# Optimization experiments

Hardware: AMD Instinct MI355X
Metric: run time of the kernel (lower is better)

## Reference

```python
import jax, jax.numpy as jnp
import numpy as np

N, E, H, HEADS, L = 10000, 64000, 128, 8, 8
D = H // HEADS
CUTOFF = 5.0
EPS = 1e-5


def _xavier(key, shape):
    lim = float(np.sqrt(6.0 / (shape[0] + shape[1])))
    return jax.random.uniform(key, shape, minval=-lim, maxval=lim, dtype=jnp.float32)


def setup_inputs() -> dict:
    key = jax.random.key(0)
    ks = jax.random.split(key, 20)
    zeros = lambda *s: jnp.zeros(s, jnp.float32)
    return {
        "x": jax.random.normal(ks[0], (N, H), jnp.float32),
        "vec": 0.1 * jax.random.normal(ks[1], (N, L, H), jnp.float32),
        "f_ij": jax.random.normal(ks[2], (E, H), jnp.float32),
        "d_ij": jax.random.normal(ks[3], (E, L), jnp.float32),
        "r_ij": jax.random.uniform(ks[4], (E,), jnp.float32, 0.0, CUTOFF),
        "edge_index": jax.random.randint(ks[5], (2, E), 0, N),
        "ln_g": jnp.ones((H,), jnp.float32), "ln_b": zeros(H),
        "vln_w": jnp.ones((H,), jnp.float32),
        "W_vec": _xavier(ks[6], (H, 3 * H)),
        "W_q": _xavier(ks[7], (H, H)), "b_q": zeros(H),
        "W_k": _xavier(ks[8], (H, H)), "b_k": zeros(H),
        "W_v": _xavier(ks[9], (H, H)), "b_v": zeros(H),
        "W_dk": _xavier(ks[10], (H, H)), "b_dk": zeros(H),
        "W_dv": _xavier(ks[11], (H, H)), "b_dv": zeros(H),
        "W_s": _xavier(ks[12], (H, 2 * H)), "b_s": zeros(2 * H),
        "W_f": _xavier(ks[13], (H, H)), "b_f": zeros(H),
        "W_src": _xavier(ks[14], (H, H)),
        "W_trg": _xavier(ks[15], (H, H)),
        "W_o": _xavier(ks[16], (H, 3 * H)), "b_o": zeros(3 * H),
    }


def _layernorm(x, g, b):
    mu = jnp.mean(x, -1, keepdims=True)
    var = jnp.mean((x - mu) ** 2, -1, keepdims=True)
    return (x - mu) * jax.lax.rsqrt(var + EPS) * g + b


def _cutoff(r):
    # CosineCutoff: 0.5*(cos(pi*r/cutoff)+1) for r < cutoff
    return 0.5 * (jnp.cos(jnp.pi * r / CUTOFF) + 1.0) * (r < CUTOFF).astype(r.dtype)


def _vec_rejection(v, d):
    # v: [E, L, H], d: [E, L]; remove the component of v along d (per channel)
    proj = jnp.einsum("elh,el->eh", v, d)
    return v - proj[:, None, :] * d[:, :, None]


def reference(x, vec, f_ij, d_ij, r_ij, edge_index, ln_g, ln_b, vln_w, W_vec,
              W_q, b_q, W_k, b_k, W_v, b_v, W_dk, b_dk, W_dv, b_dv,
              W_s, b_s, W_f, b_f, W_src, W_trg, W_o, b_o):
    src, dst = edge_index[0], edge_index[1]  # j (source), i (target)
    x = _layernorm(x, ln_g, ln_b)
    vec = vec * vln_w  # VecLayerNorm with norm_type="none": identity norm * weight

    q = (x @ W_q + b_q).reshape(N, HEADS, D)
    k = (x @ W_k + b_k).reshape(N, HEADS, D)
    v = (x @ W_v + b_v).reshape(N, HEADS, D)
    dk = jax.nn.silu(f_ij @ W_dk + b_dk).reshape(E, HEADS, D)
    dv = jax.nn.silu(f_ij @ W_dv + b_dv).reshape(E, HEADS, D)

    vec1, vec2, vec3 = jnp.split(jnp.einsum("nlh,hk->nlk", vec, W_vec), 3, axis=-1)
    vec_dot = jnp.sum(vec1 * vec2, axis=1)  # [N, H]

    # ---- message (per edge) ----
    attn = jnp.sum(q[dst] * k[src] * dk, axis=-1)          # [E, HEADS]
    attn = jax.nn.silu(attn) * _cutoff(r_ij)[:, None]
    vm = (v[src] * dv * attn[:, :, None]).reshape(E, H)    # [E, H]
    s1, s2 = jnp.split(jax.nn.silu(vm @ W_s + b_s), 2, axis=-1)
    vec_m = vec[src] * s1[:, None, :] + s2[:, None, :] * d_ij[:, :, None]  # [E, L, H]

    # ---- aggregate (scatter-add to target nodes) ----
    x_agg = jax.ops.segment_sum(vm, dst, num_segments=N)       # [N, H]
    vec_agg = jax.ops.segment_sum(vec_m, dst, num_segments=N)  # [N, L, H]

    # ---- edge update ----
    w1 = _vec_rejection(jnp.einsum("elh,hk->elk", vec[dst], W_trg), d_ij)
    w2 = _vec_rejection(jnp.einsum("elh,hk->elk", vec[src], W_src), -d_ij)
    w_dot = jnp.sum(w1 * w2, axis=1)                       # [E, H]
    df_ij = jax.nn.silu(f_ij @ W_f + b_f) * w_dot

    # ---- node update ----
    o1, o2, o3 = jnp.split(x_agg @ W_o + b_o, 3, axis=-1)
    dx = vec_dot * o2 + o3
    dvec = vec3 * o1[:, None, :] + vec_agg
    return dx, dvec, df_ij
```

## Files before the change

### kernel.cpp

```cpp
#include <hip/hip_runtime.h>
#include <hip/hip_bf16.h>
#include <math.h>

#define N_NODES 10000
#define N_EDGES 64000
#define H 128
#define L 8
#define NL (N_NODES * L)

typedef __attribute__((ext_vector_type(4))) float f32x4;
typedef __attribute__((ext_vector_type(8))) __bf16 bf16x8;
typedef __attribute__((ext_vector_type(4))) __bf16 bf16x4;

__device__ __forceinline__ float silu_f(float x) { return x / (1.f + __expf(-x)); }

__global__ __launch_bounds__(256) void ln_kernel(const float* __restrict__ x,
                                                 const float* __restrict__ g,
                                                 const float* __restrict__ b,
                                                 __bf16* __restrict__ out, int n_nodes) {
  int wave = threadIdx.x >> 6;
  int lane = threadIdx.x & 63;
  int n = blockIdx.x * 4 + wave;
  if (n >= n_nodes) return;
  const float* xr = x + (size_t)n * H;
  float a0 = xr[lane], a1 = xr[lane + 64];
  float s = a0 + a1;
#pragma unroll
  for (int off = 32; off >= 1; off >>= 1) s += __shfl_xor(s, off, 64);
  float mu = s * (1.f / H);
  float d0 = a0 - mu, d1 = a1 - mu;
  float v = d0 * d0 + d1 * d1;
#pragma unroll
  for (int off = 32; off >= 1; off >>= 1) v += __shfl_xor(v, off, 64);
  float rstd = rsqrtf(v * (1.f / H) + 1e-5f);
  __bf16* orow = out + (size_t)n * H;
  orow[lane] = (__bf16)(d0 * rstd * g[lane] + b[lane]);
  orow[lane + 64] = (__bf16)(d1 * rstd * g[lane + 64] + b[lane + 64]);
}

__global__ __launch_bounds__(256) void vecw_kernel(const float* __restrict__ vec,
                                                   const float* __restrict__ w,
                                                   __bf16* __restrict__ out,
                                                   __bf16* __restrict__ vecwT) {
  int n = blockIdx.x * 2 + (threadIdx.x >> 7);
  int h = threadIdx.x & 127;
  float wl = w[h];
  const float* base = vec + (size_t)n * 1024 + h;
  __bf16* orow = out + (size_t)n * 1024 + h;
  bf16x8 pack;
#pragma unroll
  for (int l = 0; l < 8; ++l) {
    __bf16 bv = (__bf16)(base[l * 128] * wl);
    orow[l * 128] = bv;
    pack[l] = bv;
  }
  *(bf16x8*)(vecwT + (size_t)n * 1024 + h * 8) = pack;
}

__global__ __launch_bounds__(256) void gatherf2b_kernel(const float* __restrict__ in,
                                                        const int* __restrict__ elist,
                                                        __bf16* __restrict__ out) {
  int p = blockIdx.x * 8 + (threadIdx.x >> 5);
  int c = (threadIdx.x & 31) * 4;
  int e = elist[p];
  f32x4 a = *(const f32x4*)(in + (size_t)e * 128 + c);
  bf16x4 h;
  h[0] = (__bf16)a[0]; h[1] = (__bf16)a[1]; h[2] = (__bf16)a[2]; h[3] = (__bf16)a[3];
  *(bf16x4*)(out + (size_t)p * 128 + c) = h;
}

__global__ __launch_bounds__(256) void dgather_kernel(const float* __restrict__ d_ij,
                                                      const float* __restrict__ r_ij,
                                                      const int* __restrict__ elist,
                                                      float* __restrict__ d2,
                                                      float* __restrict__ r2) {
  int idx = blockIdx.x * 256 + threadIdx.x;
  int p = idx >> 3, j = idx & 7;
  int e = elist[p];
  d2[idx] = d_ij[(size_t)e * 8 + j];
  if (j == 0) r2[p] = r_ij[e];
}

__global__ __launch_bounds__(256) void wconv_kernel(
    const float* __restrict__ Wvec, const float* __restrict__ Wq, const float* __restrict__ Wk,
    const float* __restrict__ Wv, const float* __restrict__ Wdk, const float* __restrict__ Wdv,
    const float* __restrict__ Ws, const float* __restrict__ Wtrg, const float* __restrict__ Wsrc,
    const float* __restrict__ Wf, const float* __restrict__ Wo,
    const float* __restrict__ bq, const float* __restrict__ bk, const float* __restrict__ bv,
    const float* __restrict__ bdk, const float* __restrict__ bdv, const float* __restrict__ bf,
    __bf16* __restrict__ Wt, float* __restrict__ bqkv, float* __restrict__ bfm) {
  int bid = blockIdx.x;
  int t = threadIdx.x;
  if (bid >= 256) {
    if (bid == 256) {
      if (t < 128) { bqkv[t] = bq[t]; bqkv[128 + t] = bk[t]; bqkv[256 + t] = bv[t]; }
    } else {
      if (t < 128) { bfm[t] = bdk[t]; bfm[128 + t] = bdv[t]; bfm[256 + t] = bf[t]; }
    }
    return;
  }
  int ct = bid >> 2, kt = bid & 3;
  int gc0 = ct * 32;
  const float* W; int ldw, sc0;
  if      (gc0 < 384)  { W = Wvec; ldw = 384; sc0 = gc0; }
  else if (gc0 < 512)  { W = Wtrg; ldw = 128; sc0 = gc0 - 384; }
  else if (gc0 < 640)  { W = Wsrc; ldw = 128; sc0 = gc0 - 512; }
  else if (gc0 < 768)  { W = Wq;   ldw = 128; sc0 = gc0 - 640; }
  else if (gc0 < 896)  { W = Wk;   ldw = 128; sc0 = gc0 - 768; }
  else if (gc0 < 1024) { W = Wv;   ldw = 128; sc0 = gc0 - 896; }
  else if (gc0 < 1152) { W = Wdk;  ldw = 128; sc0 = gc0 - 1024; }
  else if (gc0 < 1280) { W = Wdv;  ldw = 128; sc0 = gc0 - 1152; }
  else if (gc0 < 1408) { W = Wf;   ldw = 128; sc0 = gc0 - 1280; }
  else if (gc0 < 1664) { W = Ws;   ldw = 256; sc0 = gc0 - 1408; }
  else                 { W = Wo;   ldw = 384; sc0 = gc0 - 1664; }
  __shared__ float tile[32][33];
  int tx = t & 31, ty = t >> 5;
#pragma unroll
  for (int i = 0; i < 4; ++i)
    tile[ty + i * 8][tx] = W[(size_t)(kt * 32 + ty + i * 8) * ldw + sc0 + tx];
  __syncthreads();
#pragma unroll
  for (int i = 0; i < 4; ++i)
    Wt[(size_t)(gc0 + ty + i * 8) * 128 + kt * 32 + tx] = (__bf16)tile[tx][ty + i * 8];
}

__global__ __launch_bounds__(256, 2) void vdot_gemm(const __bf16* __restrict__ A,
                                                    const __bf16* __restrict__ Bt,
                                                    float* __restrict__ vdot) {
  __shared__ __bf16 As[128 * 128];
  const int tid = threadIdx.x;
  const int lane = tid & 63;
  const int wave = tid >> 6;
  const int wm = wave >> 1, wn = wave & 1;
  const int row0 = blockIdx.x * 128;

#pragma unroll
  for (int i = 0; i < 8; ++i) {
    int c = tid + i * 256;
    int row = c >> 4, k8 = c & 15;
    int k8s = k8 ^ (row & 7);
    const __bf16* src = A + (size_t)(row0 + row) * 128 + k8s * 8;
    __builtin_amdgcn_global_load_lds((const __attribute__((address_space(1))) void*)src,
                                     (__attribute__((address_space(3))) void*)(As + c * 8),
                                     16, 0, 0);
  }
  __syncthreads();

  f32x4 pacc[4][4], acc[4][4];
#pragma unroll
  for (int mi = 0; mi < 4; ++mi)
#pragma unroll
    for (int ni = 0; ni < 4; ++ni) {
      pacc[mi][ni] = f32x4{0.f, 0.f, 0.f, 0.f};
      acc[mi][ni] = f32x4{0.f, 0.f, 0.f, 0.f};
    }
#pragma unroll
  for (int ct = 0; ct < 2; ++ct) {
    const __bf16* Bbase =
        Bt + ((size_t)(ct * 128 + wn * 64 + (lane & 15)) << 7) + ((lane >> 4) << 3);
#pragma unroll
    for (int ks = 0; ks < 4; ++ks) {
      bf16x8 b[4];
#pragma unroll
      for (int ni = 0; ni < 4; ++ni) b[ni] = *(const bf16x8*)(Bbase + (ni << 11) + (ks << 5));
      bf16x8 a[4];
#pragma unroll
      for (int mi = 0; mi < 4; ++mi) {
        int row = wm * 64 + mi * 16 + (lane & 15);
        int byte = (row * 256 + ks * 64 + ((lane >> 4) << 4)) ^ ((row & 7) << 4);
        a[mi] = *(const bf16x8*)((const char*)As + byte);
      }
      if (ct == 0) {
#pragma unroll
        for (int mi = 0; mi < 4; ++mi)
#pragma unroll
          for (int ni = 0; ni < 4; ++ni)
            pacc[mi][ni] =
                __builtin_amdgcn_mfma_f32_16x16x32_bf16(a[mi], b[ni], pacc[mi][ni], 0, 0, 0);
      } else {
#pragma unroll
        for (int mi = 0; mi < 4; ++mi)
#pragma unroll
          for (int ni = 0; ni < 4; ++ni)
            acc[mi][ni] =
                __builtin_amdgcn_mfma_f32_16x16x32_bf16(a[mi], b[ni], acc[mi][ni], 0, 0, 0);
      }
    }
  }
#pragma unroll
  for (int mi = 0; mi < 4; ++mi) {
#pragma unroll
    for (int ni = 0; ni < 4; ++ni) {
      float sr = pacc[mi][ni][0] * acc[mi][ni][0] + pacc[mi][ni][1] * acc[mi][ni][1] +
                 pacc[mi][ni][2] * acc[mi][ni][2] + pacc[mi][ni][3] * acc[mi][ni][3];
      sr += __shfl_xor(sr, 16, 64);
      if ((lane & 16) == 0) {
        int node = (row0 >> 3) + wm * 8 + mi * 2 + (lane >> 5);
        int col = wn * 64 + ni * 16 + (lane & 15);
        vdot[(size_t)node * 128 + col] = sr;
      }
    }
  }
}

template <typename CT>
__global__ __launch_bounds__(256, 3) void gemm_v9(const __bf16* __restrict__ A,
                                                  const __bf16* __restrict__ Bt,
                                                  const float* __restrict__ bias,
                                                  CT* __restrict__ C, int M, int nx, int ny,
                                                  int ldc, int act) {
  __shared__ __bf16 As[128 * 128];
  __bf16* Cs = As;
  const int bid = blockIdx.x;
  const int xi = bid & 7;
  const int rem = bid >> 3;
  const int y = rem % ny;
  const int x = (rem / ny) * 8 + xi;
  if (x >= nx) return;
  const int tid = threadIdx.x;
  const int lane = tid & 63;
  const int wave = tid >> 6;
  const int wm = wave >> 1, wn = wave & 1;
  const int row0 = x * 128;

#pragma unroll
  for (int i = 0; i < 8; ++i) {
    int c = tid + i * 256;
    int row = c >> 4, k8 = c & 15;
    int k8s = k8 ^ (row & 7);
    const __bf16* src = A + (size_t)(row0 + row) * 128 + k8s * 8;
    __builtin_amdgcn_global_load_lds((const __attribute__((address_space(1))) void*)src,
                                     (__attribute__((address_space(3))) void*)(As + c * 8),
                                     16, 0, 0);
  }
  __syncthreads();

  const __bf16* Bbase =
      Bt + ((size_t)(y * 128 + wn * 64 + (lane & 15)) << 7) + ((lane >> 4) << 3);
  bf16x8 b[4][4];
#pragma unroll
  for (int ks = 0; ks < 4; ++ks)
#pragma unroll
    for (int ni = 0; ni < 4; ++ni) b[ks][ni] = *(const bf16x8*)(Bbase + (ni << 11) + (ks << 5));

  f32x4 acc[4][4];
#pragma unroll
  for (int mi = 0; mi < 4; ++mi)
#pragma unroll
    for (int ni = 0; ni < 4; ++ni) acc[mi][ni] = f32x4{0.f, 0.f, 0.f, 0.f};

#pragma unroll
  for (int ks = 0; ks < 4; ++ks) {
    bf16x8 a[4];
#pragma unroll
    for (int mi = 0; mi < 4; ++mi) {
      int row = wm * 64 + mi * 16 + (lane & 15);
      int byte = (row * 256 + ks * 64 + ((lane >> 4) << 4)) ^ ((row & 7) << 4);
      a[mi] = *(const bf16x8*)((const char*)As + byte);
    }
#pragma unroll
    for (int mi = 0; mi < 4; ++mi)
#pragma unroll
      for (int ni = 0; ni < 4; ++ni)
        acc[mi][ni] =
            __builtin_amdgcn_mfma_f32_16x16x32_bf16(a[mi], b[ks][ni], acc[mi][ni], 0, 0, 0);
  }

  const int cstore = y * 128;
  if constexpr (sizeof(CT) == 2) {
#pragma unroll
    for (int p = 0; p < 2; ++p) {
      __syncthreads();
      int rl = (wm << 5) | ((lane >> 4) << 2);
#pragma unroll
      for (int q = 0; q < 2; ++q) {
        int mi = 2 * p + q;
#pragma unroll
        for (int ni = 0; ni < 4; ++ni) {
          int col = wn * 64 + ni * 16 + (lane & 15);
          float bv = bias ? bias[cstore + col] : 0.f;
#pragma unroll
          for (int r = 0; r < 4; ++r) {
            float xv = acc[mi][ni][r] + bv;
            if (act) xv = silu_f(xv);
            Cs[(rl + q * 16 + r) * 136 + col] = (__bf16)xv;
          }
        }
      }
      __syncthreads();
#pragma unroll
      for (int rr = 0; rr < 4; ++rr) {
        int row = (tid >> 4) + rr * 16;
        int chunk = tid & 15;
        bf16x8 v = *(const bf16x8*)(Cs + row * 136 + chunk * 8);
        int grow = row0 + (row >> 5) * 64 + (2 * p + ((row >> 4) & 1)) * 16 + (row & 15);
        if (grow < M)
          *(bf16x8*)(C + (size_t)grow * ldc + cstore + chunk * 8) = v;
      }
    }
  } else {
#pragma unroll
    for (int mi = 0; mi < 4; ++mi) {
      int rbase = row0 + wm * 64 + mi * 16 + ((lane >> 4) << 2);
#pragma unroll
      for (int ni = 0; ni < 4; ++ni) {
        int gcol = cstore + wn * 64 + ni * 16 + (lane & 15);
        float bv = bias ? bias[cstore + wn * 64 + ni * 16 + (lane & 15)] : 0.f;
#pragma unroll
        for (int r = 0; r < 4; ++r) {
          int grow = rbase + r;
          if (grow < M) {
            float xv = acc[mi][ni][r] + bv;
            if (act) xv = silu_f(xv);
            C[(size_t)grow * ldc + gcol] = (CT)xv;
          }
        }
      }
    }
  }
}

__global__ __launch_bounds__(256, 3) void gemm_big(const __bf16* __restrict__ A,
                                                   const __bf16* __restrict__ Bt,
                                                   __bf16* __restrict__ vec3,
                                                   __bf16* __restrict__ vtT,
                                                   __bf16* __restrict__ vsT, int nx) {
  __shared__ __bf16 As[128 * 128];
  __bf16* Cs = As;
  const int bid = blockIdx.x;
  const int xi = bid & 7;
  const int rem = bid >> 3;
  const int y = rem % 3;
  const int x = (rem / 3) * 8 + xi;
  if (x >= nx) return;
  const int tid = threadIdx.x;
  const int lane = tid & 63;
  const int wave = tid >> 6;
  const int wm = wave >> 1, wn = wave & 1;
  const int row0 = x * 128;

#pragma unroll
  for (int i = 0; i < 8; ++i) {
    int c = tid + i * 256;
    int row = c >> 4, k8 = c & 15;
    int k8s = k8 ^ (row & 7);
    const __bf16* src = A + (size_t)(row0 + row) * 128 + k8s * 8;
    __builtin_amdgcn_global_load_lds((const __attribute__((address_space(1))) void*)src,
                                     (__attribute__((address_space(3))) void*)(As + c * 8),
                                     16, 0, 0);
  }
  __syncthreads();

  const __bf16* Bbase =
      Bt + ((size_t)(y * 128 + wn * 64 + (lane & 15)) << 7) + ((lane >> 4) << 3);
  bf16x8 b[4][4];
#pragma unroll
  for (int ks = 0; ks < 4; ++ks)
#pragma unroll
    for (int ni = 0; ni < 4; ++ni) b[ks][ni] = *(const bf16x8*)(Bbase + (ni << 11) + (ks << 5));

  f32x4 acc[4][4];
#pragma unroll
  for (int mi = 0; mi < 4; ++mi)
#pragma unroll
    for (int ni = 0; ni < 4; ++ni) acc[mi][ni] = f32x4{0.f, 0.f, 0.f, 0.f};

#pragma unroll
  for (int ks = 0; ks < 4; ++ks) {
    bf16x8 a[4];
#pragma unroll
    for (int mi = 0; mi < 4; ++mi) {
      int row = wm * 64 + mi * 16 + (lane & 15);
      int byte = (row * 256 + ks * 64 + ((lane >> 4) << 4)) ^ ((row & 7) << 4);
      a[mi] = *(const bf16x8*)((const char*)As + byte);
    }
#pragma unroll
    for (int mi = 0; mi < 4; ++mi)
#pragma unroll
      for (int ni = 0; ni < 4; ++ni)
        acc[mi][ni] =
            __builtin_amdgcn_mfma_f32_16x16x32_bf16(a[mi], b[ks][ni], acc[mi][ni], 0, 0, 0);
  }

  __bf16* T = (y == 1) ? vtT : vsT;
#pragma unroll
  for (int p = 0; p < 2; ++p) {
    __syncthreads();
    int rl = (wm << 5) | ((lane >> 4) << 2);
#pragma unroll
    for (int q = 0; q < 2; ++q) {
      int mi = 2 * p + q;
#pragma unroll
      for (int ni = 0; ni < 4; ++ni) {
        int col = wn * 64 + ni * 16 + (lane & 15);
#pragma unroll
        for (int r = 0; r < 4; ++r)
          Cs[(rl + q * 16 + r) * 136 + col] = (__bf16)acc[mi][ni][r];
      }
    }
    __syncthreads();
    if (y == 0) {
#pragma unroll
      for (int rr = 0; rr < 4; ++rr) {
        int row = (tid >> 4) + rr * 16;
        int chunk = tid & 15;
        bf16x8 v = *(const bf16x8*)(Cs + row * 136 + chunk * 8);
        int grow = row0 + (row >> 5) * 64 + (2 * p + ((row >> 4) & 1)) * 16 + (row & 15);
        *(bf16x8*)(vec3 + (size_t)grow * 128 + chunk * 8) = v;
      }
    } else {
#pragma unroll
      for (int j = 0; j < 4; ++j) {
        int idx = tid + 256 * j;
        int node_idx = idx >> 7;
        int h = idx & 127;
        int wmm = node_idx >> 2, qq = (node_idx >> 1) & 1, w = node_idx & 1;
        int base = wmm * 32 + qq * 16 + w * 8;
        bf16x8 v;
#pragma unroll
        for (int l = 0; l < 8; ++l) v[l] = Cs[(base + l) * 136 + h];
        int g = (row0 >> 3) + wmm * 8 + (2 * p + qq) * 2 + w;
        *(bf16x8*)(T + (size_t)g * 1024 + h * 8) = v;
      }
    }
  }
}

static inline int swz_grid(int nx, int ny) { return ((nx + 7) / 8) * ny * 8; }

__global__ __launch_bounds__(256) void msg_kernel(const __bf16* __restrict__ qkv,
                                                  const __bf16* __restrict__ fm,
                                                  const float* __restrict__ r2,
                                                  const int* __restrict__ srclist,
                                                  const int* __restrict__ dstlist,
                                                  __bf16* __restrict__ vm) {
  int p = blockIdx.x * 2 + (threadIdx.x >> 7);
  int h = threadIdx.x & 127;
  int src = srclist[p], dst = dstlist[p];
  float qv = (float)qkv[(size_t)dst * 384 + h];
  float kv = (float)qkv[(size_t)src * 384 + 128 + h];
  float vv = (float)qkv[(size_t)src * 384 + 256 + h];
  float t = qv * kv * (float)fm[(size_t)p * 384 + h];
#pragma unroll
  for (int off = 8; off >= 1; off >>= 1) t += __shfl_xor(t, off, 16);
  float r = r2[p];
  float cut = 0.5f * (__cosf(0.6283185307f * r) + 1.f);
  cut = (r < 5.f) ? cut : 0.f;
  float attn = silu_f(t) * cut;
  vm[(size_t)p * H + h] = (__bf16)(vv * (float)fm[(size_t)p * 384 + 128 + h] * attn);
}

__global__ __launch_bounds__(256) void hist_kernel(const int* __restrict__ ei,
                                                   int* __restrict__ cnt) {
  int e = blockIdx.x * 256 + threadIdx.x;
  if (e < N_EDGES) atomicAdd(&cnt[ei[N_EDGES + e]], 1);
}

__global__ __launch_bounds__(1024) void scan_kernel(const int* __restrict__ cnt,
                                                    int* __restrict__ rowptr) {
  __shared__ int wsum[16];
  int t = threadIdx.x;
  int base = t * 10;
  int local[10];
  int s = 0;
#pragma unroll
  for (int i = 0; i < 10; ++i) {
    int v = (base + i < N_NODES) ? cnt[base + i] : 0;
    local[i] = s;
    s += v;
  }
  int lane = t & 63, wave = t >> 6;
  int inc = s;
#pragma unroll
  for (int off = 1; off < 64; off <<= 1) {
    int u = __shfl_up(inc, off, 64);
    if (lane >= off) inc += u;
  }
  if (lane == 63) wsum[wave] = inc;
  __syncthreads();
  if (t == 0) {
    int acc = 0;
#pragma unroll
    for (int w = 0; w < 16; ++w) { int v = wsum[w]; wsum[w] = acc; acc += v; }
  }
  __syncthreads();
  int excl = inc - s + wsum[wave];
#pragma unroll
  for (int i = 0; i < 10; ++i)
    if (base + i <= N_NODES) rowptr[base + i] = excl + local[i];
}

__global__ __launch_bounds__(256) void fill_kernel(const int* __restrict__ ei,
                                                   const int* __restrict__ rowptr,
                                                   int* __restrict__ cursor,
                                                   int* __restrict__ elist,
                                                   int* __restrict__ srclist,
                                                   int* __restrict__ dstlist) {
  int e = blockIdx.x * 256 + threadIdx.x;
  if (e < N_EDGES) {
    int s = ei[e];
    int d = ei[N_EDGES + e];
    int p = atomicAdd(&cursor[d], 1);
    int idx = rowptr[d] + p;
    elist[idx] = e;
    srclist[idx] = s;
    dstlist[idx] = d;
  }
}

__global__ __launch_bounds__(128) void node_kernel(const __bf16* __restrict__ vm,
                                                   const __bf16* __restrict__ s,
                                                   const __bf16* __restrict__ vecwT,
                                                   const __bf16* __restrict__ vtT,
                                                   const __bf16* __restrict__ vsT,
                                                   const __bf16* __restrict__ fm,
                                                   const float* __restrict__ d2,
                                                   const int* __restrict__ srclist,
                                                   const int* __restrict__ elist,
                                                   const int* __restrict__ rowptr,
                                                   __bf16* __restrict__ x_agg,
                                                   float* __restrict__ dvec,
                                                   float* __restrict__ df) {
  int n = blockIdx.x;
  int h = threadIdx.x;
  int beg = rowptr[n], end = rowptr[n + 1];

  bf16x8 vt8 = *(const bf16x8*)(vtT + (size_t)n * 1024 + h * 8);
  float vt[L];
#pragma unroll
  for (int l = 0; l < L; l++) vt[l] = (float)vt8[l];

  float ax = 0.f;
  float av[L] = {};
  for (int p = beg; p < end; ++p) {
    int src = srclist[p];
    const float* dd = d2 + (size_t)p * L;
    float d[L], sd2 = 0.f;
#pragma unroll
    for (int l = 0; l < L; l++) {
      d[l] = dd[l];
      sd2 += d[l] * d[l];
    }
    ax += (float)vm[(size_t)p * H + h];
    float s1 = (float)s[(size_t)p * 256 + h];
    float s2 = (float)s[(size_t)p * 256 + 128 + h];
    bf16x8 vw8 = *(const bf16x8*)(vecwT + (size_t)src * 1024 + h * 8);
    bf16x8 vs8 = *(const bf16x8*)(vsT + (size_t)src * 1024 + h * 8);
    float dot = 0.f, p1 = 0.f, p2 = 0.f;
#pragma unroll
    for (int l = 0; l < L; l++) {
      av[l] += (float)vw8[l] * s1 + s2 * d[l];
      float bb = (float)vs8[l];
      dot += vt[l] * bb;
      p1 += vt[l] * d[l];
      p2 += bb * d[l];
    }
    float wdot = dot - p1 * p2 * (2.f - sd2);
    df[(size_t)elist[p] * H + h] = (float)fm[(size_t)p * 384 + 256 + h] * wdot;
  }
  x_agg[(size_t)n * H + h] = (__bf16)ax;
  float* drow = dvec + (size_t)n * L * H + h;
#pragma unroll
  for (int l = 0; l < L; l++) drow[l * H] = av[l];
}

__global__ __launch_bounds__(256) void final_kernel(const float* __restrict__ o,
                                                    const float* __restrict__ vdot,
                                                    const __bf16* __restrict__ vec3,
                                                    float* __restrict__ dx,
                                                    float* __restrict__ dvec, int n_nodes) {
  int n = blockIdx.x * 2 + (threadIdx.x >> 7);
  int h = threadIdx.x & 127;
  if (n >= n_nodes) return;
  float o1 = o[(size_t)n * 384 + h];
  float o2 = o[(size_t)n * 384 + 128 + h];
  float o3 = o[(size_t)n * 384 + 256 + h];
  dx[(size_t)n * H + h] = vdot[(size_t)n * H + h] * o2 + o3;
  float* drow = dvec + (size_t)n * L * H + h;
  const __bf16* v3 = vec3 + (size_t)n * 1024 + h;
#pragma unroll
  for (int l = 0; l < L; l++) drow[l * H] += (float)v3[l * 128] * o1;
}

extern "C" void kernel_launch(void* const* d_in, const int* in_sizes, int n_in, void* d_out,
                              int out_size, void* d_ws, size_t ws_size, hipStream_t stream) {
  const float* x = (const float*)d_in[0];
  const float* vec = (const float*)d_in[1];
  const float* f_ij = (const float*)d_in[2];
  const float* d_ij = (const float*)d_in[3];
  const float* r_ij = (const float*)d_in[4];
  const int* ei = (const int*)d_in[5];
  const float* ln_g = (const float*)d_in[6];
  const float* ln_b = (const float*)d_in[7];
  const float* vln_w = (const float*)d_in[8];
  const float* W_vec = (const float*)d_in[9];
  const float* W_q = (const float*)d_in[10];
  const float* b_q = (const float*)d_in[11];
  const float* W_k = (const float*)d_in[12];
  const float* b_k = (const float*)d_in[13];
  const float* W_v = (const float*)d_in[14];
  const float* b_v = (const float*)d_in[15];
  const float* W_dk = (const float*)d_in[16];
  const float* b_dk = (const float*)d_in[17];
  const float* W_dv = (const float*)d_in[18];
  const float* b_dv = (const float*)d_in[19];
  const float* W_s = (const float*)d_in[20];
  const float* b_s = (const float*)d_in[21];
  const float* W_f = (const float*)d_in[22];
  const float* b_f = (const float*)d_in[23];
  const float* W_src = (const float*)d_in[24];
  const float* W_trg = (const float*)d_in[25];
  const float* W_o = (const float*)d_in[26];
  const float* b_o = (const float*)d_in[27];

  float* out = (float*)d_out;
  float* dx = out;
  float* dvec = out + (size_t)N_NODES * H;
  float* df = dvec + (size_t)N_NODES * L * H;

  float* ws = (float*)d_ws;
  __bf16* vecw = (__bf16*)ws;
  __bf16* vec3 = (__bf16*)(ws + 5120000);
  __bf16* vtT = (__bf16*)(ws + 10240000);
  __bf16* vsT = (__bf16*)(ws + 15360000);
  __bf16* fm = (__bf16*)(ws + 20480000);
  __bf16* vm = (__bf16*)(ws + 32768000);
  __bf16* s_buf = (__bf16*)(ws + 36864000);
  __bf16* qkv = (__bf16*)(ws + 45056000);
  __bf16* xln = (__bf16*)(ws + 48896000);
  __bf16* xagg = (__bf16*)(ws + 49536000);
  float* vdot = ws + 50176000;
  __bf16* Wt = (__bf16*)(ws + 51456000);
  float* bqkv = ws + 51456000 + 131072;
  float* bfm = bqkv + 384;
  int* rowptr = (int*)(bfm + 384);
  int* elist = rowptr + 10001;
  int* srclist = elist + 64000;
  int* dstlist = srclist + 64000;
  int* cnt = dstlist + 64000;
  int* cursor = cnt + 10000;
  __bf16* fijb = (__bf16*)(ws + 51900000);
  __bf16* vecwT = (__bf16*)(ws + 56000000);
  float* d2 = ws + 61200000;
  float* r2 = ws + 61712000;

  float* o_buf = ws + 45056000;

  dim3 b256(256);

  hipMemsetAsync(cnt, 0, N_NODES * sizeof(int), stream);
  hipMemsetAsync(cursor, 0, N_NODES * sizeof(int), stream);
  hist_kernel<<<dim3((N_EDGES + 255) / 256), b256, 0, stream>>>(ei, cnt);
  scan_kernel<<<dim3(1), dim3(1024), 0, stream>>>(cnt, rowptr);
  fill_kernel<<<dim3((N_EDGES + 255) / 256), b256, 0, stream>>>(ei, rowptr, cursor, elist,
                                                                srclist, dstlist);
  dgather_kernel<<<dim3(N_EDGES * 8 / 256), b256, 0, stream>>>(d_ij, r_ij, elist, d2, r2);
  gatherf2b_kernel<<<dim3(N_EDGES / 8), b256, 0, stream>>>(f_ij, elist, fijb);

  wconv_kernel<<<dim3(258), b256, 0, stream>>>(W_vec, W_q, W_k, W_v, W_dk, W_dv, W_s, W_trg,
                                               W_src, W_f, W_o, b_q, b_k, b_v, b_dk, b_dv, b_f,
                                               Wt, bqkv, bfm);
  ln_kernel<<<dim3((N_NODES + 3) / 4), b256, 0, stream>>>(x, ln_g, ln_b, xln, N_NODES);
  vecw_kernel<<<dim3(N_NODES / 2), b256, 0, stream>>>(vec, vln_w, vecw, vecwT);
  vdot_gemm<<<dim3(625), b256, 0, stream>>>(vecw, Wt, vdot);
  gemm_big<<<dim3(swz_grid(625, 3)), b256, 0, stream>>>(vecw, Wt + (size_t)256 * 128, vec3,
                                                        vtT, vsT, 625);
  gemm_v9<__bf16><<<dim3(swz_grid(79, 3)), b256, 0, stream>>>(
      xln, Wt + (size_t)640 * 128, bqkv, qkv, N_NODES, 79, 3, 384, 0);
  gemm_v9<__bf16><<<dim3(swz_grid(500, 3)), b256, 0, stream>>>(
      fijb, Wt + (size_t)1024 * 128, bfm, fm, N_EDGES, 500, 3, 384, 1);
  msg_kernel<<<dim3(N_EDGES / 2), b256, 0, stream>>>(qkv, fm, r2, srclist, dstlist, vm);
  gemm_v9<__bf16><<<dim3(swz_grid(500, 2)), b256, 0, stream>>>(
      vm, Wt + (size_t)1408 * 128, b_s, s_buf, N_EDGES, 500, 2, 256, 1);
  node_kernel<<<dim3(N_NODES), dim3(128), 0, stream>>>(vm, s_buf, vecwT, vtT, vsT, fm, d2,
                                                       srclist, elist, rowptr, xagg, dvec, df);
  gemm_v9<float><<<dim3(swz_grid(79, 3)), b256, 0, stream>>>(
      xagg, Wt + (size_t)1664 * 128, b_o, o_buf, N_NODES, 79, 3, 384, 0);
  final_kernel<<<dim3(5000), b256, 0, stream>>>(o_buf, vdot, vec3, dx, dvec, N_NODES);
}
```

Baseline: 308.8 us.

## Merge small prep kernels and stage vector aggregate in bf16

Fuses layernorm with the vec-weighting kernel and the f_ij gather with the d/r gather into single launches using block-index ranges, and merges two memsets into one. The node kernel now writes its vector aggregate as packed bf16 to a scratch buffer, and the final kernel writes dvec once instead of read-modify-writing fp32. The output-projection GEMM now emits bf16. This cuts launch count and fp32 dvec traffic, at the cost of extra bf16 rounding on vec_agg and o.

```diff
diff --git a/kernel.cpp b/kernel.cpp
--- a/kernel.cpp
+++ b/kernel.cpp
@@ -14,71 +14,74 @@
 
 __device__ __forceinline__ float silu_f(float x) { return x / (1.f + __expf(-x)); }
 
-__global__ __launch_bounds__(256) void ln_kernel(const float* __restrict__ x,
-                                                 const float* __restrict__ g,
-                                                 const float* __restrict__ b,
-                                                 __bf16* __restrict__ out, int n_nodes) {
-  int wave = threadIdx.x >> 6;
-  int lane = threadIdx.x & 63;
-  int n = blockIdx.x * 4 + wave;
-  if (n >= n_nodes) return;
-  const float* xr = x + (size_t)n * H;
-  float a0 = xr[lane], a1 = xr[lane + 64];
-  float s = a0 + a1;
-#pragma unroll
-  for (int off = 32; off >= 1; off >>= 1) s += __shfl_xor(s, off, 64);
-  float mu = s * (1.f / H);
-  float d0 = a0 - mu, d1 = a1 - mu;
-  float v = d0 * d0 + d1 * d1;
-#pragma unroll
-  for (int off = 32; off >= 1; off >>= 1) v += __shfl_xor(v, off, 64);
-  float rstd = rsqrtf(v * (1.f / H) + 1e-5f);
-  __bf16* orow = out + (size_t)n * H;
-  orow[lane] = (__bf16)(d0 * rstd * g[lane] + b[lane]);
-  orow[lane + 64] = (__bf16)(d1 * rstd * g[lane + 64] + b[lane + 64]);
-}
-
-__global__ __launch_bounds__(256) void vecw_kernel(const float* __restrict__ vec,
-                                                   const float* __restrict__ w,
-                                                   __bf16* __restrict__ out,
-                                                   __bf16* __restrict__ vecwT) {
-  int n = blockIdx.x * 2 + (threadIdx.x >> 7);
-  int h = threadIdx.x & 127;
-  float wl = w[h];
-  const float* base = vec + (size_t)n * 1024 + h;
-  __bf16* orow = out + (size_t)n * 1024 + h;
-  bf16x8 pack;
-#pragma unroll
-  for (int l = 0; l < 8; ++l) {
-    __bf16 bv = (__bf16)(base[l * 128] * wl);
-    orow[l * 128] = bv;
-    pack[l] = bv;
-  }
-  *(bf16x8*)(vecwT + (size_t)n * 1024 + h * 8) = pack;
-}
-
-__global__ __launch_bounds__(256) void gatherf2b_kernel(const float* __restrict__ in,
-                                                        const int* __restrict__ elist,
-                                                        __bf16* __restrict__ out) {
-  int p = blockIdx.x * 8 + (threadIdx.x >> 5);
-  int c = (threadIdx.x & 31) * 4;
-  int e = elist[p];
-  f32x4 a = *(const f32x4*)(in + (size_t)e * 128 + c);
-  bf16x4 h;
-  h[0] = (__bf16)a[0]; h[1] = (__bf16)a[1]; h[2] = (__bf16)a[2]; h[3] = (__bf16)a[3];
-  *(bf16x4*)(out + (size_t)p * 128 + c) = h;
-}
-
-__global__ __launch_bounds__(256) void dgather_kernel(const float* __restrict__ d_ij,
+__global__ __launch_bounds__(256) void lnvecw_kernel(const float* __restrict__ x,
+                                                     const float* __restrict__ g,
+                                                     const float* __restrict__ b,
+                                                     __bf16* __restrict__ xln,
+                                                     const float* __restrict__ vec,
+                                                     const float* __restrict__ w,
+                                                     __bf16* __restrict__ vecw,
+                                                     __bf16* __restrict__ vecwT) {
+  int bid = blockIdx.x;
+  if (bid < 5000) {
+    int n = bid * 2 + (threadIdx.x >> 7);
+    int h = threadIdx.x & 127;
+    float wl = w[h];
+    const float* base = vec + (size_t)n * 1024 + h;
+    __bf16* orow = vecw + (size_t)n * 1024 + h;
+    bf16x8 pack;
+#pragma unroll
+    for (int l = 0; l < 8; ++l) {
+      __bf16 bv = (__bf16)(base[l * 128] * wl);
+      orow[l * 128] = bv;
+      pack[l] = bv;
+    }
+    *(bf16x8*)(vecwT + (size_t)n * 1024 + h * 8) = pack;
+  } else {
+    int wave = threadIdx.x >> 6;
+    int lane = threadIdx.x & 63;
+    int n = (bid - 5000) * 4 + wave;
+    if (n >= N_NODES) return;
+    const float* xr = x + (size_t)n * H;
+    float a0 = xr[lane], a1 = xr[lane + 64];
+    float s = a0 + a1;
+#pragma unroll
+    for (int off = 32; off >= 1; off >>= 1) s += __shfl_xor(s, off, 64);
+    float mu = s * (1.f / H);
+    float d0 = a0 - mu, d1 = a1 - mu;
+    float v = d0 * d0 + d1 * d1;
+#pragma unroll
+    for (int off = 32; off >= 1; off >>= 1) v += __shfl_xor(v, off, 64);
+    float rstd = rsqrtf(v * (1.f / H) + 1e-5f);
+    __bf16* orow = xln + (size_t)n * H;
+    orow[lane] = (__bf16)(d0 * rstd * g[lane] + b[lane]);
+    orow[lane + 64] = (__bf16)(d1 * rstd * g[lane + 64] + b[lane + 64]);
+  }
+}
+
+__global__ __launch_bounds__(256) void egather_kernel(const float* __restrict__ fin,
+                                                      const float* __restrict__ d_ij,
                                                       const float* __restrict__ r_ij,
                                                       const int* __restrict__ elist,
+                                                      __bf16* __restrict__ fout,
                                                       float* __restrict__ d2,
                                                       float* __restrict__ r2) {
-  int idx = blockIdx.x * 256 + threadIdx.x;
-  int p = idx >> 3, j = idx & 7;
-  int e = elist[p];
-  d2[idx] = d_ij[(size_t)e * 8 + j];
-  if (j == 0) r2[p] = r_ij[e];
+  int bid = blockIdx.x;
+  if (bid < 8000) {
+    int p = bid * 8 + (threadIdx.x >> 5);
+    int c = (threadIdx.x & 31) * 4;
+    int e = elist[p];
+    f32x4 a = *(const f32x4*)(fin + (size_t)e * 128 + c);
+    bf16x4 h;
+    h[0] = (__bf16)a[0]; h[1] = (__bf16)a[1]; h[2] = (__bf16)a[2]; h[3] = (__bf16)a[3];
+    *(bf16x4*)(fout + (size_t)p * 128 + c) = h;
+  } else {
+    int idx = (bid - 8000) * 256 + threadIdx.x;
+    int p = idx >> 3, j = idx & 7;
+    int e = elist[p];
+    d2[idx] = d_ij[(size_t)e * 8 + j];
+    if (j == 0) r2[p] = r_ij[e];
+  }
 }
 
 __global__ __launch_bounds__(256) void wconv_kernel(
@@ -519,7 +522,7 @@
                                                    const int* __restrict__ elist,
                                                    const int* __restrict__ rowptr,
                                                    __bf16* __restrict__ x_agg,
-                                                   float* __restrict__ dvec,
+                                                   __bf16* __restrict__ avb,
                                                    float* __restrict__ df) {
   int n = blockIdx.x;
   int h = threadIdx.x;
@@ -559,27 +562,30 @@
     df[(size_t)elist[p] * H + h] = (float)fm[(size_t)p * 384 + 256 + h] * wdot;
   }
   x_agg[(size_t)n * H + h] = (__bf16)ax;
-  float* drow = dvec + (size_t)n * L * H + h;
-#pragma unroll
-  for (int l = 0; l < L; l++) drow[l * H] = av[l];
-}
-
-__global__ __launch_bounds__(256) void final_kernel(const float* __restrict__ o,
+  bf16x8 pack;
+#pragma unroll
+  for (int l = 0; l < L; l++) pack[l] = (__bf16)av[l];
+  *(bf16x8*)(avb + (size_t)n * 1024 + h * 8) = pack;
+}
+
+__global__ __launch_bounds__(256) void final_kernel(const __bf16* __restrict__ o,
                                                     const float* __restrict__ vdot,
                                                     const __bf16* __restrict__ vec3,
+                                                    const __bf16* __restrict__ avb,
                                                     float* __restrict__ dx,
                                                     float* __restrict__ dvec, int n_nodes) {
   int n = blockIdx.x * 2 + (threadIdx.x >> 7);
   int h = threadIdx.x & 127;
   if (n >= n_nodes) return;
-  float o1 = o[(size_t)n * 384 + h];
-  float o2 = o[(size_t)n * 384 + 128 + h];
-  float o3 = o[(size_t)n * 384 + 256 + h];
+  float o1 = (float)o[(size_t)n * 384 + h];
+  float o2 = (float)o[(size_t)n * 384 + 128 + h];
+  float o3 = (float)o[(size_t)n * 384 + 256 + h];
   dx[(size_t)n * H + h] = vdot[(size_t)n * H + h] * o2 + o3;
+  bf16x8 av8 = *(const bf16x8*)(avb + (size_t)n * 1024 + h * 8);
   float* drow = dvec + (size_t)n * L * H + h;
   const __bf16* v3 = vec3 + (size_t)n * 1024 + h;
 #pragma unroll
-  for (int l = 0; l < L; l++) drow[l * H] += (float)v3[l * 128] * o1;
+  for (int l = 0; l < L; l++) drow[l * H] = (float)av8[l] + (float)v3[l * 128] * o1;
 }
 
 extern "C" void kernel_launch(void* const* d_in, const int* in_sizes, int n_in, void* d_out,
@@ -643,25 +649,23 @@
   __bf16* vecwT = (__bf16*)(ws + 56000000);
   float* d2 = ws + 61200000;
   float* r2 = ws + 61712000;
-
-  float* o_buf = ws + 45056000;
+  __bf16* avb = (__bf16*)(ws + 61776000);
+
+  __bf16* o_buf = qkv;
 
   dim3 b256(256);
 
-  hipMemsetAsync(cnt, 0, N_NODES * sizeof(int), stream);
-  hipMemsetAsync(cursor, 0, N_NODES * sizeof(int), stream);
+  hipMemsetAsync(cnt, 0, 2 * N_NODES * sizeof(int), stream);
   hist_kernel<<<dim3((N_EDGES + 255) / 256), b256, 0, stream>>>(ei, cnt);
   scan_kernel<<<dim3(1), dim3(1024), 0, stream>>>(cnt, rowptr);
   fill_kernel<<<dim3((N_EDGES + 255) / 256), b256, 0, stream>>>(ei, rowptr, cursor, elist,
                                                                 srclist, dstlist);
-  dgather_kernel<<<dim3(N_EDGES * 8 / 256), b256, 0, stream>>>(d_ij, r_ij, elist, d2, r2);
-  gatherf2b_kernel<<<dim3(N_EDGES / 8), b256, 0, stream>>>(f_ij, elist, fijb);
+  egather_kernel<<<dim3(8000 + 2000), b256, 0, stream>>>(f_ij, d_ij, r_ij, elist, fijb, d2, r2);
 
   wconv_kernel<<<dim3(258), b256, 0, stream>>>(W_vec, W_q, W_k, W_v, W_dk, W_dv, W_s, W_trg,
                                                W_src, W_f, W_o, b_q, b_k, b_v, b_dk, b_dv, b_f,
                                                Wt, bqkv, bfm);
-  ln_kernel<<<dim3((N_NODES + 3) / 4), b256, 0, stream>>>(x, ln_g, ln_b, xln, N_NODES);
-  vecw_kernel<<<dim3(N_NODES / 2), b256, 0, stream>>>(vec, vln_w, vecw, vecwT);
+  lnvecw_kernel<<<dim3(7500), b256, 0, stream>>>(x, ln_g, ln_b, xln, vec, vln_w, vecw, vecwT);
   vdot_gemm<<<dim3(625), b256, 0, stream>>>(vecw, Wt, vdot);
   gemm_big<<<dim3(swz_grid(625, 3)), b256, 0, stream>>>(vecw, Wt + (size_t)256 * 128, vec3,
                                                         vtT, vsT, 625);
@@ -673,8 +677,8 @@
   gemm_v9<__bf16><<<dim3(swz_grid(500, 2)), b256, 0, stream>>>(
       vm, Wt + (size_t)1408 * 128, b_s, s_buf, N_EDGES, 500, 2, 256, 1);
   node_kernel<<<dim3(N_NODES), dim3(128), 0, stream>>>(vm, s_buf, vecwT, vtT, vsT, fm, d2,
-                                                       srclist, elist, rowptr, xagg, dvec, df);
-  gemm_v9<float><<<dim3(swz_grid(79, 3)), b256, 0, stream>>>(
+                                                       srclist, elist, rowptr, xagg, avb, df);
+  gemm_v9<__bf16><<<dim3(swz_grid(79, 3)), b256, 0, stream>>>(
       xagg, Wt + (size_t)1664 * 128, b_o, o_buf, N_NODES, 79, 3, 384, 0);
-  final_kernel<<<dim3(5000), b256, 0, stream>>>(o_buf, vdot, vec3, dx, dvec, N_NODES);
-}
+  final_kernel<<<dim3(5000), b256, 0, stream>>>(o_buf, vdot, vec3, avb, dx, dvec, N_NODES);
+}
```

New measurement: 287.5 us. 1.07x faster.
